# Kernel tuning notes

Measured on AMD Instinct MI355X. Metric: run time of the kernel, lower is better.

The kernel has to match this reference:

```python
import jax, jax.numpy as jnp
import numpy as np

EMB = 1024
HEADS = 16
HEAD_DIM = EMB // HEADS
EPS = 1e-5


def layer_norm(x, scale, shift):
    mean = jnp.mean(x, axis=-1, keepdims=True)
    var = jnp.mean(jnp.square(x - mean), axis=-1, keepdims=True)  # unbiased=False
    return scale * ((x - mean) / jnp.sqrt(var + EPS)) + shift


def gelu_tanh(x):
    c = jnp.sqrt(jnp.asarray(2.0 / jnp.pi, x.dtype))
    return 0.5 * x * (1.0 + jnp.tanh(c * (x + 0.044715 * x * x * x)))


def setup_inputs() -> dict:
    key = jax.random.key(0)
    ks = jax.random.split(key, 12)
    s = 0.02
    B, S, D = 2, 2048, EMB
    return {
        "x": jax.random.normal(ks[0], (B, S, D), jnp.float32),
        "wq": jax.random.normal(ks[1], (D, D), jnp.float32) * s,
        "wk": jax.random.normal(ks[2], (D, D), jnp.float32) * s,
        "wv": jax.random.normal(ks[3], (D, D), jnp.float32) * s,
        "wo": jax.random.normal(ks[4], (D, D), jnp.float32) * s,
        "bo": jnp.zeros((D,), jnp.float32),
        "w1": jax.random.normal(ks[5], (D, 4 * D), jnp.float32) * s,
        "b1": jnp.zeros((4 * D,), jnp.float32),
        "w2": jax.random.normal(ks[6], (4 * D, D), jnp.float32) * s,
        "b2": jnp.zeros((D,), jnp.float32),
        "g1": jnp.ones((D,), jnp.float32),
        "s1": jnp.zeros((D,), jnp.float32),
        "g2": jnp.ones((D,), jnp.float32),
        "s2": jnp.zeros((D,), jnp.float32),
    }


def reference(x, wq, wk, wv, wo, bo, w1, b1, w2, b2, g1, s1, g2, s2):
    B, S, D = x.shape
    # --- attention sub-block ---
    h = layer_norm(x, g1, s1)
    q = (h @ wq).reshape(B, S, HEADS, HEAD_DIM).transpose(0, 2, 1, 3)  # [B,H,S,d]
    k = (h @ wk).reshape(B, S, HEADS, HEAD_DIM).transpose(0, 2, 1, 3)
    v = (h @ wv).reshape(B, S, HEADS, HEAD_DIM).transpose(0, 2, 1, 3)
    scores = jnp.einsum("bhqd,bhkd->bhqk", q, k)
    causal = jnp.tril(jnp.ones((S, S), bool))  # True = keep
    scores = jnp.where(causal, scores, -jnp.inf)
    attn = jax.nn.softmax(scores / jnp.sqrt(jnp.asarray(HEAD_DIM, x.dtype)), axis=-1)
    ctx = jnp.einsum("bhqk,bhkd->bhqd", attn, v).transpose(0, 2, 1, 3).reshape(B, S, D)
    x = x + (ctx @ wo + bo)
    # --- FFN sub-block ---
    h = layer_norm(x, g2, s2)
    h = gelu_tanh(h @ w1 + b1) @ w2 + b2
    return x + h
```

## Files before the change

### kernel.cpp

```cpp
#include <hip/hip_runtime.h>


typedef __attribute__((ext_vector_type(8))) short s16x8;
typedef __attribute__((ext_vector_type(4))) float f32x4;
typedef __attribute__((ext_vector_type(16))) float f32x16;
typedef unsigned short u16;
typedef unsigned int u32;

#define DEV static __device__ __forceinline__
#define MFMA16 __builtin_amdgcn_mfma_f32_16x16x32_bf16
#define MFMA32 __builtin_amdgcn_mfma_f32_32x32x16_bf16
#define GLOAD_LDS16(gp, lp)                                         \
  __builtin_amdgcn_global_load_lds(                                 \
      (const __attribute__((address_space(1))) void*)(gp),          \
      (__attribute__((address_space(3))) void*)(lp), 16, 0, 0)
#define WAIT_VM(N) asm volatile("s_waitcnt vmcnt(" #N ")" ::: "memory")

DEV u16 f2bf(float f) {
  union { float f; unsigned u; } c; c.f = f;
  unsigned u = c.u;
  u += 0x7fff + ((u >> 16) & 1);
  return (u16)(u >> 16);
}

DEV u32 cvtpk(float lo, float hi) {
  u32 r;
  asm("v_cvt_pk_bf16_f32 %0, %1, %2" : "=v"(r) : "v"(lo), "v"(hi));
  return r;
}

DEV float frcp(float x) {
  float r;
  asm("v_rcp_f32 %0, %1" : "=v"(r) : "v"(x));
  return r;
}

DEV float gelu_tanh(float v) {
  const float K = -2.3021171648f;
  const float a = 0.044715f;
  const float w = v * v;
  const float q = fmaf(a, w, 1.0f);
  const float z = exp2f(K * v * q);
  return v * frcp(1.0f + z);
}

DEV s16x8 ld8(const u16* p) { return *(const s16x8*)p; }

DEV void tconv_tile(const float* __restrict__ W, u16* __restrict__ Wt, int K,
                    int N, int bx, int by, int t) {
  __shared__ u16 T[64][80];
  const int n0 = bx * 64, k0 = by * 64;
  const int kr = t >> 4, nc = (t & 15) * 4;
#pragma unroll
  for (int p = 0; p < 4; ++p) {
    const int k = p * 16 + kr;
    float4 v = *(const float4*)(W + (size_t)(k0 + k) * N + n0 + nc);
    T[nc + 0][k] = f2bf(v.x);
    T[nc + 1][k] = f2bf(v.y);
    T[nc + 2][k] = f2bf(v.z);
    T[nc + 3][k] = f2bf(v.w);
  }
  __syncthreads();
  const int nr = t >> 2, kc = (t & 3) * 16;
  *(s16x8*)(Wt + (size_t)(n0 + nr) * K + k0 + kc) = *(const s16x8*)&T[nr][kc];
  *(s16x8*)(Wt + (size_t)(n0 + nr) * K + k0 + kc + 8) =
      *(const s16x8*)&T[nr][kc + 8];
}

__global__ __launch_bounds__(256) void tconv_all(
    const float* __restrict__ wq, const float* __restrict__ wk,
    const float* __restrict__ wv, const float* __restrict__ wo,
    const float* __restrict__ w1, const float* __restrict__ w2,
    u16* __restrict__ qkvw, u16* __restrict__ wot, u16* __restrict__ w1t,
    u16* __restrict__ w2t) {
  const int idx = blockIdx.x, t = threadIdx.x;
  if (idx < 768) {
    const int which = idx >> 8, r = idx & 255;
    const float* W = which == 0 ? wq : (which == 1 ? wk : wv);
    tconv_tile(W, qkvw + which * 1048576, 1024, 1024, r & 15, r >> 4, t);
  } else if (idx < 1024) {
    const int r = idx - 768;
    tconv_tile(wo, wot, 1024, 1024, r & 15, r >> 4, t);
  } else if (idx < 2048) {
    const int r = idx - 1024;
    tconv_tile(w1, w1t, 1024, 4096, r & 63, r >> 6, t);
  } else {
    const int r = idx - 2048;
    tconv_tile(w2, w2t, 4096, 1024, r & 15, r >> 4, t);
  }
}

__global__ __launch_bounds__(256) void ln_kernel(
    const float* __restrict__ x, const float* __restrict__ g,
    const float* __restrict__ b, u16* __restrict__ out) {
  const int row = blockIdx.x;
  const int t = threadIdx.x;
  const float* xr = x + (size_t)row * 1024;
  float4 v = *(const float4*)(xr + t * 4);
  float s = v.x + v.y + v.z + v.w;
  float ss = v.x * v.x + v.y * v.y + v.z * v.z + v.w * v.w;
#pragma unroll
  for (int off = 1; off < 64; off <<= 1) {
    s += __shfl_xor(s, off);
    ss += __shfl_xor(ss, off);
  }
  __shared__ float sb[4], ssb[4];
  const int w = t >> 6;
  if ((t & 63) == 0) { sb[w] = s; ssb[w] = ss; }
  __syncthreads();
  s = sb[0] + sb[1] + sb[2] + sb[3];
  ss = ssb[0] + ssb[1] + ssb[2] + ssb[3];
  const float mean = s * (1.0f / 1024.0f);
  const float var = ss * (1.0f / 1024.0f) - mean * mean;
  const float rstd = rsqrtf(var + 1e-5f);
  const int c = t * 4;
  ushort4 o;
  o.x = f2bf(g[c + 0] * ((v.x - mean) * rstd) + b[c + 0]);
  o.y = f2bf(g[c + 1] * ((v.y - mean) * rstd) + b[c + 1]);
  o.z = f2bf(g[c + 2] * ((v.z - mean) * rstd) + b[c + 2]);
  o.w = f2bf(g[c + 3] * ((v.w - mean) * rstd) + b[c + 3]);
  *(ushort4*)(out + (size_t)row * 1024 + c) = o;
}

DEV void stage128(const u16* __restrict__ A, const u16* __restrict__ Bt,
                  int bm, int bn, int K, int kof, u16 (*Al)[32],
                  u16 (*Bl)[32], int w, int lane) {
  const int srow = lane >> 2;
  const int scol = ((lane & 3) ^ ((lane >> 3) & 3)) * 8;
#pragma unroll
  for (int p = 0; p < 2; ++p) {
    const int r0 = (w * 2 + p) * 16;
    GLOAD_LDS16(A + (size_t)(bm + r0 + srow) * K + kof + scol, &Al[r0][0]);
    GLOAD_LDS16(Bt + (size_t)(bn + r0 + srow) * K + kof + scol, &Bl[r0][0]);
  }
}

DEV void step128(const u16 (*Al)[32], const u16 (*Bl)[32],
                 f32x4 (&acc)[4][4], int wm, int wn, int lr, int lg) {
  const int cs = (lg ^ ((lr >> 1) & 3)) * 8;
  s16x8 af[4], bf[4];
#pragma unroll
  for (int i = 0; i < 4; ++i) {
    af[i] = *(const s16x8*)&Al[wm + i * 16 + lr][cs];
    bf[i] = *(const s16x8*)&Bl[wn + i * 16 + lr][cs];
  }
#pragma unroll
  for (int i = 0; i < 4; ++i)
#pragma unroll
    for (int j = 0; j < 4; ++j)
      acc[i][j] = MFMA16(af[i], bf[j], acc[i][j], 0, 0, 0);
}

template <int EPI>
__global__ __launch_bounds__(256) void pipe128_kernel(
    const u16* __restrict__ A, const u16* __restrict__ Bt,
    const float* __restrict__ bias, const float* __restrict__ res,
    void* __restrict__ Cv, int M, int N, int K) {
  __shared__ __align__(16) u16 Al[3][128][32];
  __shared__ __align__(16) u16 Bl[3][128][32];
  const int t = threadIdx.x;
  const int lane = t & 63, w = t >> 6;
  const int wm = (w >> 1) * 64, wn = (w & 1) * 64;
  int bid = blockIdx.y * gridDim.x + blockIdx.x;
  const int q8 = (gridDim.x * gridDim.y) >> 3;
  bid = (bid & 7) * q8 + (bid >> 3);
  const int bm = (bid / gridDim.x) * 128, bn = (bid % gridDim.x) * 128;
  const int lr = lane & 15, lg = lane >> 4;
  f32x4 acc[4][4] = {};
  const int nkt = K >> 5;

  stage128(A, Bt, bm, bn, K, 0, Al[0], Bl[0], w, lane);
  stage128(A, Bt, bm, bn, K, 32, Al[1], Bl[1], w, lane);
  for (int kt = 0; kt < nkt; ++kt) {
    if (kt == nkt - 1) WAIT_VM(0);
    else               WAIT_VM(4);
    __builtin_amdgcn_s_barrier();
    if (kt + 2 < nkt) {
      const int nb = (kt + 2) % 3;
      stage128(A, Bt, bm, bn, K, (kt + 2) << 5, Al[nb], Bl[nb], w, lane);
    }
    step128(Al[kt % 3], Bl[kt % 3], acc, wm, wn, lr, lg);
  }

#pragma unroll
  for (int i = 0; i < 4; ++i) {
    const int row = bm + wm + i * 16 + lg * 4;
#pragma unroll
    for (int j = 0; j < 4; ++j) {
      const int col = bn + wn + j * 16 + lr;
      if (EPI == 0) {
        const int bb = row >> 11, sloc = row & 2047;
        const int which = col >> 10, n = col & 1023;
        const int hh = n >> 6, dd = n & 63;
        u16* qbuf = (u16*)Cv;
        if (which == 2) {
          ushort4 o;
          o.x = f2bf(acc[i][j][0]); o.y = f2bf(acc[i][j][1]);
          o.z = f2bf(acc[i][j][2]); o.w = f2bf(acc[i][j][3]);
          *(ushort4*)(qbuf + 8388608 +
                      (size_t)((bb * 16 + hh) * 64 + dd) * 2048 + sloc) = o;
        } else {
          const float sc = (which == 0) ? 0.18033688011112042f : 1.0f;
          u16* dst = qbuf + (size_t)which * 4194304 +
                     ((size_t)(bb * 16 + hh) * 2048 + sloc) * 64 + dd;
#pragma unroll
          for (int e = 0; e < 4; ++e) dst[(size_t)e * 64] = f2bf(acc[i][j][e] * sc);
        }
      } else {
        u16* C = (u16*)Cv;
        const float bs = bias[col];
#pragma unroll
        for (int e = 0; e < 4; ++e)
          C[(size_t)(row + e) * N + col] = f2bf(gelu_tanh(acc[i][j][e] + bs));
      }
    }
  }
}

DEV void stage64(const u16* __restrict__ A, const u16* __restrict__ Bt,
                 int bm, int bn, int K, int kof, u16 (*Al)[32],
                 u16 (*Bl)[32], int w, int lane) {
  const int srow = lane >> 2;
  const int scol = ((lane & 3) ^ ((lane >> 3) & 3)) * 8;
  const int r0 = w << 4;
  GLOAD_LDS16(A + (size_t)(bm + r0 + srow) * K + kof + scol, &Al[r0][0]);
  GLOAD_LDS16(Bt + (size_t)(bn + r0 + srow) * K + kof + scol, &Bl[r0][0]);
}

DEV void step64(const u16 (*Al)[32], const u16 (*Bl)[32],
                f32x4 (&acc)[2][2], int wm, int wn, int lr, int lg) {
  const int cs = (lg ^ ((lr >> 1) & 3)) * 8;
  s16x8 af[2], bf[2];
#pragma unroll
  for (int i = 0; i < 2; ++i) {
    af[i] = *(const s16x8*)&Al[wm + i * 16 + lr][cs];
    bf[i] = *(const s16x8*)&Bl[wn + i * 16 + lr][cs];
  }
#pragma unroll
  for (int i = 0; i < 2; ++i)
#pragma unroll
    for (int j = 0; j < 2; ++j)
      acc[i][j] = MFMA16(af[i], bf[j], acc[i][j], 0, 0, 0);
}

__global__ __launch_bounds__(256) void pipe64_kernel(
    const u16* __restrict__ A, const u16* __restrict__ Bt,
    const float* __restrict__ bias, const float* __restrict__ res,
    float* __restrict__ C, int M, int N, int K) {
  __shared__ __align__(16) u16 Al[3][64][32];
  __shared__ __align__(16) u16 Bl[3][64][32];
  const int t = threadIdx.x;
  const int lane = t & 63, w = t >> 6;
  const int wm = (w >> 1) * 32, wn = (w & 1) * 32;
  int bid = blockIdx.y * gridDim.x + blockIdx.x;
  const int q8 = (gridDim.x * gridDim.y) >> 3;
  bid = (bid & 7) * q8 + (bid >> 3);
  const int bm = (bid / gridDim.x) * 64, bn = (bid % gridDim.x) * 64;
  const int lr = lane & 15, lg = lane >> 4;
  f32x4 acc[2][2] = {};
  const int nkt = K >> 5;

  stage64(A, Bt, bm, bn, K, 0, Al[0], Bl[0], w, lane);
  stage64(A, Bt, bm, bn, K, 32, Al[1], Bl[1], w, lane);
  for (int kt = 0; kt < nkt; ++kt) {
    if (kt == nkt - 1) WAIT_VM(0);
    else               WAIT_VM(2);
    __builtin_amdgcn_s_barrier();
    if (kt + 2 < nkt) {
      const int nb = (kt + 2) % 3;
      stage64(A, Bt, bm, bn, K, (kt + 2) << 5, Al[nb], Bl[nb], w, lane);
    }
    step64(Al[kt % 3], Bl[kt % 3], acc, wm, wn, lr, lg);
  }

#pragma unroll
  for (int i = 0; i < 2; ++i) {
    const int row = bm + wm + i * 16 + lg * 4;
#pragma unroll
    for (int j = 0; j < 2; ++j) {
      const int col = bn + wn + j * 16 + lr;
      const float bs = bias[col];
#pragma unroll
      for (int e = 0; e < 4; ++e)
        C[(size_t)(row + e) * N + col] =
            acc[i][j][e] + bs + res[(size_t)(row + e) * N + col];
    }
  }
}

DEV float vsum16(const f32x16& v) {
  float a = v[0] + v[1], b = v[2] + v[3];
  float c = v[4] + v[5], d = v[6] + v[7];
  float e = v[8] + v[9], f = v[10] + v[11];
  float g = v[12] + v[13], h = v[14] + v[15];
  a += b; c += d; e += f; g += h;
  return (a + c) + (e + g);
}

struct A32 {
  s16x8 q[4];
  f32x16 o0, o1;
  float l;
};

struct TileRegs { s16x8 k0[4], k1[4], v0[4], v1[4]; };

DEV void tld(TileRegs& r, int k0, const u16* Kb, const u16* Vb, int la,
             int hi) {
#pragma unroll
  for (int c = 0; c < 4; ++c) {
    r.k0[c] = ld8(Kb + (size_t)(k0 + la) * 64 + c * 16 + hi * 8);
    r.k1[c] = ld8(Kb + (size_t)(k0 + 32 + la) * 64 + c * 16 + hi * 8);
    r.v0[c] = ld8(Vb + (size_t)la * 2048 + k0 + c * 16 + hi * 8);
    r.v1[c] = ld8(Vb + (size_t)(32 + la) * 2048 + k0 + c * 16 + hi * 8);
  }
}

DEV void pv_accum(A32& st, const s16x8* v0, const s16x8* v1,
                  const f32x16& s0, const f32x16& s1, int nh, int hi) {
#pragma unroll
  for (int half = 0; half < 2; ++half) {
    if (half >= nh) break;
    u32 w[8];
#pragma unroll
    for (int i = 0; i < 8; ++i)
      w[i] = half ? cvtpk(s1[2 * i], s1[2 * i + 1])
                  : cvtpk(s0[2 * i], s0[2 * i + 1]);
#pragma unroll
    for (int kp = 0; kp < 2; ++kp) {
      const u32 w0 = w[4 * kp + 0], w1 = w[4 * kp + 1];
      const u32 w2 = w[4 * kp + 2], w3 = w[4 * kp + 3];
      const u32 t0 = hi ? w0 : w2, t1 = hi ? w1 : w3;
      const u32 x0 = (u32)__shfl_xor((int)t0, 32);
      const u32 x1 = (u32)__shfl_xor((int)t1, 32);
      union { u32 u[4]; s16x8 v; } bb;
      bb.u[0] = hi ? x0 : w0;
      bb.u[1] = hi ? x1 : w1;
      bb.u[2] = hi ? w2 : x0;
      bb.u[3] = hi ? w3 : x1;
      const int kc = half * 2 + kp;
      st.o0 = MFMA32(v0[kc], bb.v, st.o0, 0, 0, 0);
      st.o1 = MFMA32(v1[kc], bb.v, st.o1, 0, 0, 0);
    }
  }
}

DEV void bcomp0(A32& st, const TileRegs& tr, int la, int hi) {
  f32x16 s0, s1;
#pragma unroll
  for (int r = 0; r < 16; ++r) { s0[r] = 0.f; s1[r] = 0.f; }
#pragma unroll
  for (int c = 0; c < 4; ++c) s0 = MFMA32(tr.k0[c], st.q[c], s0, 0, 0, 0);
#pragma unroll
  for (int c = 0; c < 4; ++c) s1 = MFMA32(tr.k1[c], st.q[c], s1, 0, 0, 0);
#pragma unroll
  for (int r = 0; r < 16; ++r) s0[r] = exp2f(s0[r] - 2.0f);
#pragma unroll
  for (int r = 0; r < 16; ++r) s1[r] = exp2f(s1[r] - 2.0f);
  float rs = vsum16(s0) + vsum16(s1);
  rs += __shfl_xor(rs, 32);
  st.l += rs;
  pv_accum(st, tr.v0, tr.v1, s0, s1, 2, hi);
}

template <int MODE>
DEV void body32(A32& st, int k0, const u16* Kb, const u16* Vb, int la,
                int hi) {
  s16x8 ka0[4], ka1[4];
#pragma unroll
  for (int c = 0; c < 4; ++c)
    ka0[c] = ld8(Kb + (size_t)(k0 + la) * 64 + c * 16 + hi * 8);
  if (MODE != 2)
#pragma unroll
    for (int c = 0; c < 4; ++c)
      ka1[c] = ld8(Kb + (size_t)(k0 + 32 + la) * 64 + c * 16 + hi * 8);
  f32x16 s0, s1;
#pragma unroll
  for (int r = 0; r < 16; ++r) { s0[r] = 0.f; s1[r] = 0.f; }
#pragma unroll
  for (int c = 0; c < 4; ++c) s0 = MFMA32(ka0[c], st.q[c], s0, 0, 0, 0);
  if (MODE != 2)
#pragma unroll
    for (int c = 0; c < 4; ++c) s1 = MFMA32(ka1[c], st.q[c], s1, 0, 0, 0);
  const int nkc = (MODE == 2) ? 2 : 4;
  s16x8 va0[4], va1[4];
#pragma unroll
  for (int kc = 0; kc < 4; ++kc)
    if (kc < nkc) {
      va0[kc] = ld8(Vb + (size_t)la * 2048 + k0 + kc * 16 + hi * 8);
      va1[kc] = ld8(Vb + (size_t)(32 + la) * 2048 + k0 + kc * 16 + hi * 8);
    }
  if (MODE == 1) {
#pragma unroll
    for (int r = 0; r < 16; ++r) {
      const int kl = (r & 3) + 8 * (r >> 2) + 4 * hi;
      if (kl > la) s1[r] = -INFINITY;
    }
  }
  if (MODE == 2) {
#pragma unroll
    for (int r = 0; r < 16; ++r) {
      const int kl = (r & 3) + 8 * (r >> 2) + 4 * hi;
      if (kl > la) s0[r] = -INFINITY;
    }
  }
#pragma unroll
  for (int r = 0; r < 16; ++r) s0[r] = exp2f(s0[r] - 2.0f);
  if (MODE != 2)
#pragma unroll
    for (int r = 0; r < 16; ++r) s1[r] = exp2f(s1[r] - 2.0f);
  float rs = vsum16(s0);
  if (MODE != 2) rs += vsum16(s1);
  rs += __shfl_xor(rs, 32);
  st.l += rs;
  pv_accum(st, va0, va1, s0, s1, (MODE == 2) ? 1 : 2, hi);
}

DEV void a32_init(A32& st, const u16* Qbase, int qs, int la, int hi) {
#pragma unroll
  for (int c = 0; c < 4; ++c)
    st.q[c] = ld8(Qbase + (size_t)(qs + la) * 64 + c * 16 + hi * 8);
#pragma unroll
  for (int r = 0; r < 16; ++r) { st.o0[r] = 0.f; st.o1[r] = 0.f; }
  st.l = 0.f;
}

DEV void a32_fin(const A32& st, u16* __restrict__ ctx, int bh, int qs, int la,
                 int hi) {
  const int bb = bh >> 4, hh = bh & 15;
  const float inv = 1.0f / st.l;
  u16* crow = ctx + (size_t)(bb * 2048 + qs + la) * 1024 + hh * 64;
#pragma unroll
  for (int r = 0; r < 16; r += 2) {
    const int d = (r & 3) + 8 * (r >> 2) + 4 * hi;
    *(u32*)(crow + d) = cvtpk(st.o0[r] * inv, st.o0[r + 1] * inv);
    *(u32*)(crow + 32 + d) = cvtpk(st.o1[r] * inv, st.o1[r + 1] * inv);
  }
}

__global__ __launch_bounds__(64) void attn_kernel(
    const u16* __restrict__ Qg, const u16* __restrict__ Kg,
    const u16* __restrict__ Vt, u16* __restrict__ ctx) {
  const int lane = threadIdx.x & 63;
  const int la = lane & 31, hi = lane >> 5;
  const int bid = blockIdx.x;
  const int j = bid >> 3;
  const int bh = ((j >> 5) << 3) | (bid & 7);
  const int tA = j & 31;
  const int tB = 63 - tA;
  const int qsA = tA * 32, qsB = tB * 32;
  const int nfA = tA >> 1, nfB = tB >> 1;
  const size_t baseK = (size_t)bh * 2048 * 64;
  const size_t baseV = (size_t)bh * 64 * 2048;
  const u16* Kb = Kg + baseK;
  const u16* Vb = Vt + baseV;

  A32 A, B;
  a32_init(A, Qg + baseK, qsA, la, hi);
  a32_init(B, Qg + baseK, qsB, la, hi);

  TileRegs r0, r1;
  tld(r0, 0, Kb, Vb, la, hi);
  int kt = 0;
  while (kt < nfB) {
    if (kt + 1 < nfB) tld(r1, (kt + 1) * 64, Kb, Vb, la, hi);
    bcomp0(B, r0, la, hi);
    if (kt < nfA) bcomp0(A, r0, la, hi);
    ++kt;
    if (kt >= nfB) break;
    if (kt + 1 < nfB) tld(r0, (kt + 1) * 64, Kb, Vb, la, hi);
    bcomp0(B, r1, la, hi);
    if (kt < nfA) bcomp0(A, r1, la, hi);
    ++kt;
  }

  if (tA & 1) body32<1>(A, nfA * 64, Kb, Vb, la, hi);
  else        body32<2>(A, nfA * 64, Kb, Vb, la, hi);
  if (tB & 1) body32<1>(B, nfB * 64, Kb, Vb, la, hi);
  else        body32<2>(B, nfB * 64, Kb, Vb, la, hi);
  a32_fin(A, ctx, bh, qsA, la, hi);
  a32_fin(B, ctx, bh, qsB, la, hi);
}

extern "C" void kernel_launch(void* const* d_in, const int* in_sizes, int n_in,
                              void* d_out, int out_size, void* d_ws,
                              size_t ws_size, hipStream_t stream) {
  const float* x  = (const float*)d_in[0];
  const float* wq = (const float*)d_in[1];
  const float* wk = (const float*)d_in[2];
  const float* wv = (const float*)d_in[3];
  const float* wo = (const float*)d_in[4];
  const float* bo = (const float*)d_in[5];
  const float* w1 = (const float*)d_in[6];
  const float* b1 = (const float*)d_in[7];
  const float* w2 = (const float*)d_in[8];
  const float* b2 = (const float*)d_in[9];
  const float* g1 = (const float*)d_in[10];
  const float* s1 = (const float*)d_in[11];
  const float* g2 = (const float*)d_in[12];
  const float* s2 = (const float*)d_in[13];
  float* out = (float*)d_out;

  const size_t MB = (size_t)1 << 20;
  char* p = (char*)d_ws;
  u16* hb    = (u16*)(p + 0 * MB);
  u16* qbuf  = (u16*)(p + 8 * MB);
  u16* ctxb  = (u16*)(p + 32 * MB);
  float* x2  = (float*)(p + 40 * MB);
  u16* h2b   = (u16*)(p + 56 * MB);
  u16* qkvw  = (u16*)(p + 64 * MB);
  u16* wot   = (u16*)(p + 70 * MB);
  u16* w1t   = (u16*)(p + 72 * MB);
  u16* w2t   = (u16*)(p + 80 * MB);
  u16* gb    = (u16*)(p + 0 * MB);

  const dim3 blk(256);
  tconv_all<<<dim3(3072), blk, 0, stream>>>(wq, wk, wv, wo, w1, w2, qkvw, wot,
                                            w1t, w2t);
  ln_kernel<<<4096, blk, 0, stream>>>(x, g1, s1, hb);
  pipe128_kernel<0><<<dim3(24, 32), blk, 0, stream>>>(
      hb, qkvw, nullptr, nullptr, qbuf, 4096, 3072, 1024);
  attn_kernel<<<dim3(1024), dim3(64), 0, stream>>>(
      qbuf, qbuf + 4194304, qbuf + 8388608, ctxb);
  pipe64_kernel<<<dim3(16, 64), blk, 0, stream>>>(ctxb, wot, bo, x, x2, 4096,
                                                  1024, 1024);
  ln_kernel<<<4096, blk, 0, stream>>>(x2, g2, s2, h2b);
  pipe128_kernel<2><<<dim3(32, 32), blk, 0, stream>>>(
      h2b, w1t, b1, nullptr, gb, 4096, 4096, 1024);
  pipe64_kernel<<<dim3(16, 64), blk, 0, stream>>>(gb, w2t, b2, x2, out, 4096,
                                                  1024, 4096);
}
```

Baseline: 265.0 us.

## Enlarge QKV and FFN1 GEMM tiles to 256x256 with 512-thread blocks

Replaces the 128x128 GEMM kernel used for the QKV projection and the first FFN matmul with a 256x256 tile version. It runs 8 waves per block, each wave holding a 128x64 accumulator in 8x4 MFMA 16x16 fragments. The goal is more operand reuse per LDS read and less global traffic per output. The cost is higher register and LDS use per block (96KB of triple-buffered LDS) and far fewer blocks: 192 for QKV and 256 for FFN1. That may leave compute units idle and hurt latency hiding.

Result: slower. 274.5 us (+3.6%).

```diff
diff --git a/kernel.cpp b/kernel.cpp
--- a/kernel.cpp
+++ b/kernel.cpp
@@ -122,7 +122,7 @@
   *(ushort4*)(out + (size_t)row * 1024 + c) = o;
 }
 
-DEV void stage128(const u16* __restrict__ A, const u16* __restrict__ Bt,
+DEV void stage256(const u16* __restrict__ A, const u16* __restrict__ Bt,
                   int bm, int bn, int K, int kof, u16 (*Al)[32],
                   u16 (*Bl)[32], int w, int lane) {
   const int srow = lane >> 2;
@@ -135,55 +135,56 @@
   }
 }
 
-DEV void step128(const u16 (*Al)[32], const u16 (*Bl)[32],
-                 f32x4 (&acc)[4][4], int wm, int wn, int lr, int lg) {
+DEV void step256(const u16 (*Al)[32], const u16 (*Bl)[32],
+                 f32x4 (&acc)[8][4], int wm, int wn, int lr, int lg) {
   const int cs = (lg ^ ((lr >> 1) & 3)) * 8;
-  s16x8 af[4], bf[4];
-#pragma unroll
-  for (int i = 0; i < 4; ++i) {
+  s16x8 af[8], bf[4];
+#pragma unroll
+  for (int i = 0; i < 8; ++i)
     af[i] = *(const s16x8*)&Al[wm + i * 16 + lr][cs];
-    bf[i] = *(const s16x8*)&Bl[wn + i * 16 + lr][cs];
-  }
-#pragma unroll
-  for (int i = 0; i < 4; ++i)
+#pragma unroll
+  for (int j = 0; j < 4; ++j)
+    bf[j] = *(const s16x8*)&Bl[wn + j * 16 + lr][cs];
+#pragma unroll
+  for (int i = 0; i < 8; ++i)
 #pragma unroll
     for (int j = 0; j < 4; ++j)
       acc[i][j] = MFMA16(af[i], bf[j], acc[i][j], 0, 0, 0);
 }
 
 template <int EPI>
-__global__ __launch_bounds__(256) void pipe128_kernel(
+__global__ __launch_bounds__(512, 2) void pipe256_kernel(
     const u16* __restrict__ A, const u16* __restrict__ Bt,
-    const float* __restrict__ bias, const float* __restrict__ res,
-    void* __restrict__ Cv, int M, int N, int K) {
-  __shared__ __align__(16) u16 Al[3][128][32];
-  __shared__ __align__(16) u16 Bl[3][128][32];
+    const float* __restrict__ bias, void* __restrict__ Cv, int M, int N,
+    int K) {
+  __shared__ __align__(16) u16 Al[3][256][32];
+  __shared__ __align__(16) u16 Bl[3][256][32];
   const int t = threadIdx.x;
   const int lane = t & 63, w = t >> 6;
-  const int wm = (w >> 1) * 64, wn = (w & 1) * 64;
+  const int wm = (w >> 2) * 128, wn = (w & 3) * 64;
   int bid = blockIdx.y * gridDim.x + blockIdx.x;
   const int q8 = (gridDim.x * gridDim.y) >> 3;
   bid = (bid & 7) * q8 + (bid >> 3);
-  const int bm = (bid / gridDim.x) * 128, bn = (bid % gridDim.x) * 128;
+  const int bm = (bid / gridDim.x) * 256, bn = (bid % gridDim.x) * 256;
   const int lr = lane & 15, lg = lane >> 4;
-  f32x4 acc[4][4] = {};
+  f32x4 acc[8][4] = {};
   const int nkt = K >> 5;
 
-  stage128(A, Bt, bm, bn, K, 0, Al[0], Bl[0], w, lane);
-  stage128(A, Bt, bm, bn, K, 32, Al[1], Bl[1], w, lane);
+  stage256(A, Bt, bm, bn, K, 0, Al[0], Bl[0], w, lane);
+  stage256(A, Bt, bm, bn, K, 32, Al[1], Bl[1], w, lane);
   for (int kt = 0; kt < nkt; ++kt) {
     if (kt == nkt - 1) WAIT_VM(0);
     else               WAIT_VM(4);
     __builtin_amdgcn_s_barrier();
     if (kt + 2 < nkt) {
       const int nb = (kt + 2) % 3;
-      stage128(A, Bt, bm, bn, K, (kt + 2) << 5, Al[nb], Bl[nb], w, lane);
-    }
-    step128(Al[kt % 3], Bl[kt % 3], acc, wm, wn, lr, lg);
-  }
-
-#pragma unroll
-  for (int i = 0; i < 4; ++i) {
+      stage256(A, Bt, bm, bn, K, (kt + 2) << 5, Al[nb], Bl[nb], w, lane);
+    }
+    step256(Al[kt % 3], Bl[kt % 3], acc, wm, wn, lr, lg);
+  }
+
+#pragma unroll
+  for (int i = 0; i < 8; ++i) {
     const int row = bm + wm + i * 16 + lg * 4;
 #pragma unroll
     for (int j = 0; j < 4; ++j) {
@@ -518,15 +519,15 @@
   tconv_all<<<dim3(3072), blk, 0, stream>>>(wq, wk, wv, wo, w1, w2, qkvw, wot,
                                             w1t, w2t);
   ln_kernel<<<4096, blk, 0, stream>>>(x, g1, s1, hb);
-  pipe128_kernel<0><<<dim3(24, 32), blk, 0, stream>>>(
-      hb, qkvw, nullptr, nullptr, qbuf, 4096, 3072, 1024);
+  pipe256_kernel<0><<<dim3(12, 16), dim3(512), 0, stream>>>(
+      hb, qkvw, nullptr, qbuf, 4096, 3072, 1024);
   attn_kernel<<<dim3(1024), dim3(64), 0, stream>>>(
       qbuf, qbuf + 4194304, qbuf + 8388608, ctxb);
   pipe64_kernel<<<dim3(16, 64), blk, 0, stream>>>(ctxb, wot, bo, x, x2, 4096,
                                                   1024, 1024);
   ln_kernel<<<4096, blk, 0, stream>>>(x2, g2, s2, h2b);
-  pipe128_kernel<2><<<dim3(32, 32), blk, 0, stream>>>(
-      h2b, w1t, b1, nullptr, gb, 4096, 4096, 1024);
+  pipe256_kernel<2><<<dim3(16, 16), dim3(512), 0, stream>>>(
+      h2b, w1t, b1, gb, 4096, 4096, 1024);
   pipe64_kernel<<<dim3(16, 64), blk, 0, stream>>>(gb, w2t, b2, x2, out, 4096,
                                                   1024, 4096);
 }
```
